# Kernel optimization log

Hardware: AMD Instinct MI355X
Metric: run time of the kernel (lower is better)

## Reference

```python
import jax, jax.numpy as jnp
import numpy as np

B, L, E, H, RR, BIO, NT, V, R = 16, 128, 256, 256, 128, 64, 3, 30000, 25


def setup_inputs() -> dict:
    key = jax.random.key(0)
    ks = jax.random.split(key, 24)
    s = 0.05
    n = jax.random.normal
    inp = {
        'tokens': jax.random.randint(ks[0], (B, L), 0, V),
        'bio_gold': jax.random.randint(ks[1], (B, L), 0, NT),
        'selection_gold': jax.random.uniform(ks[2], (B, L, R, L), jnp.float32),
        'word_emb': n(ks[3], (V, E), jnp.float32) * s,
        'W_ih_f': n(ks[4], (4 * H, E), jnp.float32) * s,
        'W_hh_f': n(ks[5], (4 * H, H), jnp.float32) * s,
        'b_f': n(ks[6], (4 * H,), jnp.float32) * s,
        'W_ih_b': n(ks[7], (4 * H, E), jnp.float32) * s,
        'W_hh_b': n(ks[8], (4 * H, H), jnp.float32) * s,
        'b_b': n(ks[9], (4 * H,), jnp.float32) * s,
        'emi_W': n(ks[10], (NT, H), jnp.float32) * s,
        'emi_b': n(ks[11], (NT,), jnp.float32) * s,
        'bio_emb': n(ks[12], (NT + 1, BIO), jnp.float32) * s,
        'sel_u_W': n(ks[13], (RR, H + BIO), jnp.float32) * s,
        'sel_u_b': n(ks[14], (RR,), jnp.float32) * s,
        'sel_v_W': n(ks[15], (RR, H + BIO), jnp.float32) * s,
        'sel_v_b': n(ks[16], (RR,), jnp.float32) * s,
        'sel_uv_W': n(ks[17], (RR, 2 * RR), jnp.float32) * s,
        'sel_uv_b': n(ks[18], (RR,), jnp.float32) * s,
        'rel_emb': n(ks[19], (R, RR), jnp.float32) * s,
        'crf_start': n(ks[20], (NT,), jnp.float32) * s,
        'crf_end': n(ks[21], (NT,), jnp.float32) * s,
        'crf_trans': n(ks[22], (NT, NT), jnp.float32) * s,
    }
    return inp


def _lstm(x, W_ih, W_hh, b, reverse):
    # x: [B,L,E] -> hidden states [B,L,H]; PyTorch gate order i,f,g,o
    Bb = x.shape[0]
    Hh = W_hh.shape[1]
    xg = jnp.swapaxes(jnp.einsum('ble,ge->blg', x, W_ih) + b, 0, 1)  # [L,B,4H]

    def step(carry, xt):
        h, c = carry
        g = xt + h @ W_hh.T
        i, f, gg, o = jnp.split(g, 4, axis=-1)
        c = jax.nn.sigmoid(f) * c + jax.nn.sigmoid(i) * jnp.tanh(gg)
        h = jax.nn.sigmoid(o) * jnp.tanh(c)
        return (h, c), h

    init = (jnp.zeros((Bb, Hh), x.dtype), jnp.zeros((Bb, Hh), x.dtype))
    _, hs = jax.lax.scan(step, init, xg, reverse=reverse)
    return jnp.swapaxes(hs, 0, 1)


def reference(tokens, bio_gold, selection_gold, word_emb, W_ih_f, W_hh_f, b_f,
              W_ih_b, W_hh_b, b_b, emi_W, emi_b, bio_emb, sel_u_W, sel_u_b,
              sel_v_W, sel_v_b, sel_uv_W, sel_uv_b, rel_emb, crf_start,
              crf_end, crf_trans):
    mask = tokens != 0  # pad id 0
    maskf = mask.astype(jnp.float32)
    emb = word_emb[tokens]
    # BiLSTM, halves averaged as in (fwd + bwd) / 2
    o = (_lstm(emb, W_ih_f, W_hh_f, b_f, False)
         + _lstm(emb, W_ih_b, W_hh_b, b_b, True)) * 0.5
    emi = o @ emi_W.T + emi_b  # [B,L,NT]

    # ---- CRF negative log-likelihood (torchcrf, reduction='mean') ----
    bidx = jnp.arange(tokens.shape[0])
    e_sel = jnp.take_along_axis(emi, bio_gold[..., None], axis=2)[..., 0]  # [B,L]
    num = crf_start[bio_gold[:, 0]] + e_sel[:, 0]
    tr = crf_trans[bio_gold[:, :-1], bio_gold[:, 1:]]  # [B,L-1]
    num = num + ((tr + e_sel[:, 1:]) * maskf[:, 1:]).sum(1)
    seq_ends = jnp.maximum(mask.sum(1) - 1, 0)
    num = num + crf_end[bio_gold[bidx, seq_ends]]

    def crf_step(score, inp):
        emi_t, m_t = inp
        nxt = jax.nn.logsumexp(score[:, :, None] + crf_trans[None] + emi_t[:, None, :], axis=1)
        return jnp.where(m_t[:, None], nxt, score), None

    score0 = crf_start + emi[:, 0]
    score, _ = jax.lax.scan(crf_step, score0,
                            (jnp.swapaxes(emi[:, 1:], 0, 1), jnp.swapaxes(mask[:, 1:], 0, 1)))
    den = jax.nn.logsumexp(score + crf_end, axis=1)
    crf_loss = -(num - den).mean()

    # ---- pairwise biaffine selection head ----
    oc = jnp.concatenate([o, bio_emb[bio_gold]], axis=-1)  # [B,L,H+BIO]
    u = jax.nn.relu(oc @ sel_u_W.T + sel_u_b)  # [B,L,RR]
    v = jax.nn.relu(oc @ sel_v_W.T + sel_v_b)
    Rr = rel_emb.shape[1]
    W1, W2 = sel_uv_W[:, :Rr], sel_uv_W[:, Rr:]  # split cat([u,v]) linear
    a = u @ W1.T  # indexed by j (u was expanded along dim 1)
    c = v @ W2.T  # indexed by i
    uv = jax.nn.relu(a[:, None, :, :] + c[:, :, None, :] + sel_uv_b)  # [B,L,L,RR]
    logits = jnp.einsum('bijh,rh->birj', uv, rel_emb)  # [B,L,R,L]

    y = selection_gold
    bce = jnp.maximum(logits, 0) - logits * y + jnp.log1p(jnp.exp(-jnp.abs(logits)))
    selmask = maskf[:, :, None, None] * maskf[:, None, None, :]  # [B,L,1,L]
    sel_loss = (bce * selmask).sum() / maskf.sum()
    return crf_loss + sel_loss
```

## Files before the change

kernel.cpp:

```cpp
#include <hip/hip_runtime.h>
#include <cstdint>
#include <cstddef>


typedef __attribute__((ext_vector_type(8))) short short8;
typedef __attribute__((ext_vector_type(8))) int i32x8;
typedef __attribute__((ext_vector_type(4))) float f32x4;

__device__ __forceinline__ unsigned short f2bf(float f) {
  unsigned int u = __float_as_uint(f);
  u += 0x7fffu + ((u >> 16) & 1u);
  return (unsigned short)(u >> 16);
}
__device__ __forceinline__ float bf2f(unsigned short u) {
  return __uint_as_float(((unsigned int)u) << 16);
}

__device__ __forceinline__ void dev_pp8k128(const float* __restrict__ W,
                                            unsigned int* __restrict__ out, int idx) {
  int c = idx & 3;
  int lane = (idx >> 2) & 63;
  int f = idx >> 8;
  int nt = f >> 1, kt = f & 1;
  int n = nt * 16 + (lane & 15);
  int k0 = kt * 128 + (lane >> 4) * 32 + c * 8;
  const float* wp = &W[(size_t)n * 256 + k0];
  int lo = 0, hi = 0;
  lo = __builtin_amdgcn_cvt_pk_fp8_f32(wp[0], wp[1], lo, false);
  lo = __builtin_amdgcn_cvt_pk_fp8_f32(wp[2], wp[3], lo, true);
  hi = __builtin_amdgcn_cvt_pk_fp8_f32(wp[4], wp[5], hi, false);
  hi = __builtin_amdgcn_cvt_pk_fp8_f32(wp[6], wp[7], hi, true);
  size_t base = ((size_t)(f << 6) + lane) * 8 + (c << 1);
  out[base] = (unsigned)lo;
  out[base + 1] = (unsigned)hi;
}

__device__ __forceinline__ void dev_ppw(const float* __restrict__ W, int ldw, int nkt,
                                        uint4* __restrict__ out, int idx) {
  int lane = idx & 63;
  int f = idx >> 6;
  int kt = f % nkt;
  int nt = f / nkt;
  int row = nt * 16 + (lane & 15);
  int k0 = kt * 32 + ((lane >> 4) << 3);
  const float* wp = &W[(size_t)row * ldw + k0];
  union { unsigned short us[8]; uint4 v; } tmp;
#pragma unroll
  for (int j = 0; j < 8; ++j) tmp.us[j] = f2bf(wp[j]);
  out[idx] = tmp.v;
}

__global__ __launch_bounds__(256) void k_setup(
    const float* __restrict__ Whhf, unsigned int* __restrict__ wpk8f,
    const float* __restrict__ Whhb, unsigned int* __restrict__ wpk8b,
    const float* __restrict__ Wihf, uint4* __restrict__ wihfPk,
    const float* __restrict__ Wihb, uint4* __restrict__ wihbPk,
    const float* __restrict__ suW, uint4* __restrict__ suPk,
    const float* __restrict__ svW, uint4* __restrict__ svPk,
    const float* __restrict__ suvW, uint4* __restrict__ w1Pk, uint4* __restrict__ w2Pk,
    float* __restrict__ acc) {
  int bid = blockIdx.x;
  int t = threadIdx.x;
  if (bid < 128) {
    dev_pp8k128(Whhf, wpk8f, bid * 256 + t);
  } else if (bid < 256) {
    dev_pp8k128(Whhb, wpk8b, (bid - 128) * 256 + t);
  } else if (bid < 384) {
    dev_ppw(Wihf, 256, 8, wihfPk, (bid - 256) * 256 + t);
  } else if (bid < 512) {
    dev_ppw(Wihb, 256, 8, wihbPk, (bid - 384) * 256 + t);
  } else if (bid < 532) {
    dev_ppw(suW, 320, 10, suPk, (bid - 512) * 256 + t);
  } else if (bid < 552) {
    dev_ppw(svW, 320, 10, svPk, (bid - 532) * 256 + t);
  } else if (bid < 560) {
    dev_ppw(suvW, 256, 4, w1Pk, (bid - 552) * 256 + t);
  } else if (bid < 568) {
    dev_ppw(suvW + 128, 256, 4, w2Pk, (bid - 560) * 256 + t);
  } else {
    if (t < 16) acc[t] = 0.f;
  }
}

__global__ __launch_bounds__(256) void k_xg(
    const int* __restrict__ tok, const float* __restrict__ wemb,
    const uint4* __restrict__ WpkF, const float* __restrict__ biasF,
    unsigned short* __restrict__ CF,
    const uint4* __restrict__ WpkB, const float* __restrict__ biasB,
    unsigned short* __restrict__ CB) {
  const uint4* Wp = blockIdx.z ? WpkB : WpkF;
  const float* bi = blockIdx.z ? biasB : biasF;
  unsigned short* Co = blockIdx.z ? CB : CF;
  int bn = blockIdx.x, bm = blockIdx.y;
  int tid = threadIdx.x;
  int w = tid >> 6;
  int lane = tid & 63;
  int m = lane & 15;
  int q = lane >> 4;
  int arow = bm * 64 + w * 16 + m;
  const float* ew = wemb + (size_t)tok[arow] * 256 + (q << 3);
  f32x4 z = {0.f, 0.f, 0.f, 0.f};
  f32x4 ac[4] = {z, z, z, z};
  for (int kt = 0; kt < 8; ++kt) {
    float4 e0 = *reinterpret_cast<const float4*>(ew + (kt << 5));
    float4 e1 = *reinterpret_cast<const float4*>(ew + (kt << 5) + 4);
    union { unsigned short us[8]; short8 v; } af;
    af.us[0] = f2bf(e0.x); af.us[1] = f2bf(e0.y); af.us[2] = f2bf(e0.z); af.us[3] = f2bf(e0.w);
    af.us[4] = f2bf(e1.x); af.us[5] = f2bf(e1.y); af.us[6] = f2bf(e1.z); af.us[7] = f2bf(e1.w);
#pragma unroll
    for (int nt = 0; nt < 4; ++nt) {
      uint4 b4 = Wp[(size_t)(((bn << 2) + nt) * 8 + kt) * 64 + lane];
      ac[nt] = __builtin_amdgcn_mfma_f32_16x16x32_bf16(af.v, __builtin_bit_cast(short8, b4), ac[nt], 0, 0, 0);
    }
  }
#pragma unroll
  for (int nt = 0; nt < 4; ++nt) {
    int col = (bn << 6) + (nt << 4) + m;
    float bv = bi[col];
#pragma unroll
    for (int reg = 0; reg < 4; ++reg) {
      int row = (bm << 6) + (w << 4) + (q << 2) + reg;
      Co[(size_t)row * 1024 + col] = f2bf(ac[nt][reg] + bv);
    }
  }
}

__global__ __launch_bounds__(1024, 4) void k_lstm8(
    const unsigned short* __restrict__ xgf, const unsigned short* __restrict__ xgb,
    const unsigned int* __restrict__ wpkf, const unsigned int* __restrict__ wpkb,
    unsigned short* __restrict__ hsf, unsigned short* __restrict__ hsb) {
  int bid = blockIdx.x;
  int dir = bid >> 4;
  int b = bid & 15;
  const unsigned short* xg = (dir ? xgb : xgf) + (size_t)b * 128 * 1024;
  const unsigned int* wpk = dir ? wpkb : wpkf;
  unsigned short* hseq = (dir ? hsb : hsf) + (size_t)b * 128 * 256;

  __shared__ __align__(16) unsigned short xgl[8 * 1024];
  __shared__ __align__(16) unsigned short hfl[8 * 256];
  __shared__ __align__(16) unsigned char h8[2][256];

  int tid = threadIdx.x;
  int w = tid >> 6;
  int lane = tid & 63;
  int m = lane & 15;
  int q = lane >> 4;

  i32x8 wfr[4][2];
#pragma unroll
  for (int g = 0; g < 4; ++g)
#pragma unroll
    for (int kt = 0; kt < 2; ++kt) {
      int f = (((g << 4) + w) << 1) + kt;
      wfr[g][kt] = *reinterpret_cast<const i32x8*>(wpk + (((size_t)(f << 6) + lane) << 3));
    }
#pragma unroll
  for (int g = 0; g < 4; ++g)
#pragma unroll
    for (int kt = 0; kt < 2; ++kt)
      asm volatile("" : "+v"(wfr[g][kt]));

  if (tid < 128) reinterpret_cast<unsigned int*>(&h8[0][0])[tid] = 0u;
  {
    int tb0 = dir ? 120 : 0;
    uint4 x0v = *reinterpret_cast<const uint4*>((const char*)xg + (size_t)tb0 * 2048 + tid * 16);
    reinterpret_cast<uint4*>(xgl)[tid] = x0v;
  }
  __syncthreads();

  float cstate = 0.f;
  int j = (w << 4) + m;

  for (int c = 0; c < 16; ++c) {
    int tbase = dir ? (120 - 8 * c) : (8 * c);
    uint4 xnext = {0, 0, 0, 0};
    if (c < 15) {
      int tb2 = dir ? (tbase - 8) : (tbase + 8);
      xnext = *reinterpret_cast<const uint4*>((const char*)xg + (size_t)tb2 * 2048 + tid * 16);
    }
#pragma unroll
    for (int i = 0; i < 8; ++i) {
      int s = 8 * c + i;
      int t = dir ? (127 - s) : s;
      int slot = t & 7;
      const unsigned char* cur = h8[s & 1];
      unsigned char* nxt = h8[(s & 1) ^ 1];

      const unsigned short* xb = xgl + slot * 1024 + j;
      float x0 = bf2f(xb[0]);
      float x1 = bf2f(xb[256]);
      float x2 = bf2f(xb[512]);
      float x3 = bf2f(xb[768]);

      i32x8 afr[2];
#pragma unroll
      for (int kt = 0; kt < 2; ++kt) {
        union { uint4 u[2]; i32x8 v; } tmp;
        const unsigned char* hp = cur + kt * 128 + q * 32;
        tmp.u[0] = *reinterpret_cast<const uint4*>(hp);
        tmp.u[1] = *reinterpret_cast<const uint4*>(hp + 16);
        afr[kt] = tmp.v;
      }

      f32x4 acg[4];
      acg[0] = (f32x4){x0, 0.f, 0.f, 0.f};
      acg[1] = (f32x4){x1, 0.f, 0.f, 0.f};
      acg[2] = (f32x4){x2, 0.f, 0.f, 0.f};
      acg[3] = (f32x4){x3, 0.f, 0.f, 0.f};
#pragma unroll
      for (int kt = 0; kt < 2; ++kt)
#pragma unroll
        for (int g = 0; g < 4; ++g)
          acg[g] = __builtin_amdgcn_mfma_scale_f32_16x16x128_f8f6f4(
              afr[kt], wfr[g][kt], acg[g],
              0, 0, 0, 0x7f7f7f7f, 0, 0x7f7f7f7f);

      float gi = acg[0][0];
      float gf = acg[1][0];
      float gg = acg[2][0];
      float go = acg[3][0];
      float si = __fdividef(1.f, 1.f + __expf(-gi));
      float sf = __fdividef(1.f, 1.f + __expf(-gf));
      float so = __fdividef(1.f, 1.f + __expf(-go));
      float tg = 1.f - __fdividef(2.f, __expf(2.f * gg) + 1.f);
      float cc2 = sf * cstate + si * tg;
      cstate = cc2;
      float th = 1.f - __fdividef(2.f, __expf(2.f * cc2) + 1.f);
      float h = so * th;
      if (q == 0) {
        hfl[slot * 256 + j] = f2bf(h);
        int pk = __builtin_amdgcn_cvt_pk_fp8_f32(h, h, 0, false);
        nxt[j] = (unsigned char)(pk & 0xff);
      }
      asm volatile("s_waitcnt lgkmcnt(0)" ::: "memory");
      __builtin_amdgcn_s_barrier();
      asm volatile("" ::: "memory");
    }
    if (tid < 256) {
      int trow = tid >> 5;
      int j0 = (tid & 31) << 3;
      uint4 hv = reinterpret_cast<const uint4*>(hfl)[tid];
      *reinterpret_cast<uint4*>(hseq + (size_t)(tbase + trow) * 256 + j0) = hv;
    }
    if (c < 15) {
      reinterpret_cast<uint4*>(xgl)[tid] = xnext;
      __syncthreads();
    }
  }
}

__global__ __launch_bounds__(256) void k_mid2(
    const unsigned short* __restrict__ hf16, const unsigned short* __restrict__ hb16,
    const int* __restrict__ bio, const float* __restrict__ bioE,
    const float* __restrict__ emiW, const float* __restrict__ emib,
    const uint4* __restrict__ suPk, const float* __restrict__ sub,
    const uint4* __restrict__ svPk, const float* __restrict__ svb,
    const uint4* __restrict__ w1Pk, const uint4* __restrict__ w2Pk,
    unsigned short* __restrict__ a16, unsigned short* __restrict__ c16,
    float* __restrict__ emi) {
  __shared__ __align__(16) unsigned short oc[16][328];
  __shared__ __align__(16) unsigned short ub[16][136];
  __shared__ __align__(16) unsigned short vb[16][136];
  int r0 = blockIdx.x * 16;
  int tid = threadIdx.x;

#pragma unroll
  for (int it = 0; it < 8; ++it) {
    int i = it * 256 + tid;
    int row = i >> 7, h2 = (i & 127) << 1;
    unsigned int af = *reinterpret_cast<const unsigned int*>(hf16 + (size_t)(r0 + row) * 256 + h2);
    unsigned int ab = *reinterpret_cast<const unsigned int*>(hb16 + (size_t)(r0 + row) * 256 + h2);
    float lo = 0.5f * (bf2f((unsigned short)af) + bf2f((unsigned short)ab));
    float hi = 0.5f * (bf2f((unsigned short)(af >> 16)) + bf2f((unsigned short)(ab >> 16)));
    unsigned int pk = (unsigned int)f2bf(lo) | ((unsigned int)f2bf(hi) << 16);
    *reinterpret_cast<unsigned int*>(&oc[row][h2]) = pk;
  }
#pragma unroll
  for (int it = 0; it < 2; ++it) {
    int i = it * 256 + tid;
    int row = i >> 5, p = (i & 31) << 1;
    int bi = bio[r0 + row];
    float b0 = bioE[bi * 64 + p], b1 = bioE[bi * 64 + p + 1];
    unsigned int pk = (unsigned int)f2bf(b0) | ((unsigned int)f2bf(b1) << 16);
    *reinterpret_cast<unsigned int*>(&oc[row][256 + p]) = pk;
  }
  __syncthreads();

  if (tid < 192) {
    int did = tid >> 2, sub4 = tid & 3;
    int row = did / 3, g = did - row * 3;
    const float* ew = emiW + g * 256 + sub4 * 64;
    float av = 0.f;
#pragma unroll
    for (int k = 0; k < 64; ++k) av += bf2f(oc[row][sub4 * 64 + k]) * ew[k];
    av += __shfl_xor(av, 1);
    av += __shfl_xor(av, 2);
    if (sub4 == 0) emi[(size_t)(r0 + row) * 3 + g] = av + emib[g];
  }

  int w = tid >> 6, lane = tid & 63, m = lane & 15, q = lane >> 4;
  {
    f32x4 z = {0.f, 0.f, 0.f, 0.f};
    f32x4 au[2] = {z, z}, av2[2] = {z, z};
    for (int kt = 0; kt < 10; ++kt) {
      uint4 a4 = *reinterpret_cast<const uint4*>(&oc[m][(kt << 5) + (q << 3)]);
      short8 af = __builtin_bit_cast(short8, a4);
#pragma unroll
      for (int d = 0; d < 2; ++d) {
        int nt = (w << 1) + d;
        uint4 bu = suPk[(size_t)(nt * 10 + kt) * 64 + lane];
        uint4 bv = svPk[(size_t)(nt * 10 + kt) * 64 + lane];
        au[d] = __builtin_amdgcn_mfma_f32_16x16x32_bf16(af, __builtin_bit_cast(short8, bu), au[d], 0, 0, 0);
        av2[d] = __builtin_amdgcn_mfma_f32_16x16x32_bf16(af, __builtin_bit_cast(short8, bv), av2[d], 0, 0, 0);
      }
    }
#pragma unroll
    for (int d = 0; d < 2; ++d) {
      int col = ((w << 1) + d) * 16 + m;
      float bu = sub[col], bv = svb[col];
#pragma unroll
      for (int reg = 0; reg < 4; ++reg) {
        int row = (q << 2) + reg;
        ub[row][col] = f2bf(fmaxf(au[d][reg] + bu, 0.f));
        vb[row][col] = f2bf(fmaxf(av2[d][reg] + bv, 0.f));
      }
    }
  }
  __syncthreads();

  {
    f32x4 z = {0.f, 0.f, 0.f, 0.f};
    f32x4 aa[2] = {z, z}, cc[2] = {z, z};
    for (int kt = 0; kt < 4; ++kt) {
      uint4 ua = *reinterpret_cast<const uint4*>(&ub[m][(kt << 5) + (q << 3)]);
      uint4 va = *reinterpret_cast<const uint4*>(&vb[m][(kt << 5) + (q << 3)]);
      short8 uf = __builtin_bit_cast(short8, ua);
      short8 vf = __builtin_bit_cast(short8, va);
#pragma unroll
      for (int d = 0; d < 2; ++d) {
        int nt = (w << 1) + d;
        uint4 b1 = w1Pk[(size_t)((nt << 2) + kt) * 64 + lane];
        uint4 b2 = w2Pk[(size_t)((nt << 2) + kt) * 64 + lane];
        aa[d] = __builtin_amdgcn_mfma_f32_16x16x32_bf16(uf, __builtin_bit_cast(short8, b1), aa[d], 0, 0, 0);
        cc[d] = __builtin_amdgcn_mfma_f32_16x16x32_bf16(vf, __builtin_bit_cast(short8, b2), cc[d], 0, 0, 0);
      }
    }
#pragma unroll
    for (int d = 0; d < 2; ++d) {
      int col = ((w << 1) + d) * 16 + m;
#pragma unroll
      for (int reg = 0; reg < 4; ++reg) {
        int row = r0 + (q << 2) + reg;
        a16[(size_t)row * 128 + col] = f2bf(aa[d][reg]);
        c16[(size_t)row * 128 + col] = f2bf(cc[d][reg]);
      }
    }
  }
}

__global__ __launch_bounds__(256) void k_loss(
    const unsigned short* __restrict__ a16, const unsigned short* __restrict__ c16,
    const float* __restrict__ suvb, const float* __restrict__ rel,
    const float* __restrict__ y, const int* __restrict__ tok,
    const float* __restrict__ emi, const int* __restrict__ bio,
    const float* __restrict__ cstart, const float* __restrict__ cend,
    const float* __restrict__ ctrans,
    float* __restrict__ acc, float* __restrict__ out) {
  int blk = blockIdx.x;
  int tid = threadIdx.x;
  if (blk < 1024) {
    __shared__ unsigned short alds[128][136];
    __shared__ float cbs[2][128];
    __shared__ float red[4];
    int b = blk >> 6;
    int ip = blk & 63;
    int hh = tid & 127;
    int half = tid >> 7;
#pragma unroll
    for (int it = 0; it < 32; ++it) {
      int idx = it * 256 + tid;
      int jrow = idx >> 6;
      int h2 = (idx & 63) << 1;
      unsigned int av = *reinterpret_cast<const unsigned int*>(
          a16 + ((size_t)(b << 7) + jrow) * 128 + h2);
      alds[h2][jrow] = (unsigned short)av;
      alds[h2 + 1][jrow] = (unsigned short)(av >> 16);
    }
    {
      int i = (ip << 1) + half;
      cbs[half][hh] = bf2f(c16[(size_t)((b << 7) + i) * 128 + hh]) + suvb[hh];
    }
    __syncthreads();
    int i = (ip << 1) + half;
    int j = hh;
    float lg[25];
#pragma unroll
    for (int r = 0; r < 25; ++r) lg[r] = 0.f;
    for (int h = 0; h < 128; ++h) {
      float av = bf2f(alds[h][j]);
      float uv = fmaxf(av + cbs[half][h], 0.f);
#pragma unroll
      for (int r = 0; r < 25; ++r) lg[r] += uv * rel[r * 128 + h];
    }
    float mi = (tok[(b << 7) + i] != 0) ? 1.f : 0.f;
    float mj = (tok[(b << 7) + j] != 0) ? 1.f : 0.f;
    const float* yp = y + (size_t)((b << 7) + i) * 3200 + j;
    float bs = 0.f;
#pragma unroll
    for (int r = 0; r < 25; ++r) {
      float x = lg[r];
      float yv = yp[r * 128];
      bs += fmaxf(x, 0.f) - x * yv + __logf(1.f + __expf(-fabsf(x)));
    }
    bs *= mi * mj;
#pragma unroll
    for (int off = 32; off; off >>= 1) bs += __shfl_down(bs, off);
    if ((tid & 63) == 0) red[tid >> 6] = bs;
    __syncthreads();
    if (tid == 0) atomicAdd(&acc[0], red[0] + red[1] + red[2] + red[3]);
  } else {
    __shared__ float elds[128][4];
    __shared__ float msk[128];
    __shared__ int biol[128];
    __shared__ float r_t[2], r_m[2];
    int b = blk - 1024;
    int t = tid;
    if (t < 128) {
      biol[t] = bio[b * 128 + t];
      msk[t] = (tok[b * 128 + t] != 0) ? 1.f : 0.f;
#pragma unroll
      for (int g = 0; g < 3; ++g) elds[t][g] = emi[(b * 128 + t) * 3 + g];
    }
    __syncthreads();
    if (t < 128) {
      float m = msk[t];
      float term;
      if (t == 0)
        term = cstart[biol[0]] + elds[0][biol[0]];
      else
        term = (ctrans[biol[t - 1] * 3 + biol[t]] + elds[t][biol[t]]) * m;
      float ms = m;
#pragma unroll
      for (int off = 32; off; off >>= 1) {
        term += __shfl_down(term, off);
        ms += __shfl_down(ms, off);
      }
      if ((t & 63) == 0) { r_t[t >> 6] = term; r_m[t >> 6] = ms; }
    }
    __syncthreads();
    if (t == 0) {
      float num = r_t[0] + r_t[1];
      float msum = r_m[0] + r_m[1];
      int se = (int)msum - 1;
      if (se < 0) se = 0;
      num += cend[biol[se]];
      float tr[9];
#pragma unroll
      for (int i2 = 0; i2 < 9; ++i2) tr[i2] = ctrans[i2];
      float s0 = cstart[0] + elds[0][0];
      float s1 = cstart[1] + elds[0][1];
      float s2 = cstart[2] + elds[0][2];
      for (int tt = 1; tt < 128; ++tt) {
        float a0, a1, a2, mx, n0, n1, n2;
        a0 = s0 + tr[0]; a1 = s1 + tr[3]; a2 = s2 + tr[6];
        mx = fmaxf(a0, fmaxf(a1, a2));
        n0 = mx + __logf(__expf(a0 - mx) + __expf(a1 - mx) + __expf(a2 - mx)) + elds[tt][0];
        a0 = s0 + tr[1]; a1 = s1 + tr[4]; a2 = s2 + tr[7];
        mx = fmaxf(a0, fmaxf(a1, a2));
        n1 = mx + __logf(__expf(a0 - mx) + __expf(a1 - mx) + __expf(a2 - mx)) + elds[tt][1];
        a0 = s0 + tr[2]; a1 = s1 + tr[5]; a2 = s2 + tr[8];
        mx = fmaxf(a0, fmaxf(a1, a2));
        n2 = mx + __logf(__expf(a0 - mx) + __expf(a1 - mx) + __expf(a2 - mx)) + elds[tt][2];
        if (msk[tt] != 0.f) { s0 = n0; s1 = n1; s2 = n2; }
      }
      float a0 = s0 + cend[0], a1 = s1 + cend[1], a2 = s2 + cend[2];
      float mx = fmaxf(a0, fmaxf(a1, a2));
      float den = mx + __logf(__expf(a0 - mx) + __expf(a1 - mx) + __expf(a2 - mx));
      atomicAdd(&acc[1], num - den);
      atomicAdd(&acc[2], msum);
    }
  }
  if (tid == 0) {
    __threadfence();
    unsigned old = atomicAdd((unsigned int*)(acc + 5), 1u);
    if (old == 1039u) {
      __threadfence();
      float s0 = atomicAdd(&acc[0], 0.f);
      float s1 = atomicAdd(&acc[1], 0.f);
      float s2 = atomicAdd(&acc[2], 0.f);
      out[0] = -(s1 * (1.f / 16.f)) + s0 / s2;
    }
  }
}

extern "C" void kernel_launch(void* const* d_in, const int* in_sizes, int n_in,
                              void* d_out, int out_size, void* d_ws, size_t ws_size,
                              hipStream_t stream) {
  const int* tokens = (const int*)d_in[0];
  const int* bio = (const int*)d_in[1];
  const float* selg = (const float*)d_in[2];
  const float* wemb = (const float*)d_in[3];
  const float* Wihf = (const float*)d_in[4];
  const float* Whhf = (const float*)d_in[5];
  const float* bf = (const float*)d_in[6];
  const float* Wihb = (const float*)d_in[7];
  const float* Whhb = (const float*)d_in[8];
  const float* bb = (const float*)d_in[9];
  const float* emiW = (const float*)d_in[10];
  const float* emib = (const float*)d_in[11];
  const float* bioE = (const float*)d_in[12];
  const float* suW = (const float*)d_in[13];
  const float* sub = (const float*)d_in[14];
  const float* svW = (const float*)d_in[15];
  const float* svb = (const float*)d_in[16];
  const float* suvW = (const float*)d_in[17];
  const float* suvb = (const float*)d_in[18];
  const float* rel = (const float*)d_in[19];
  const float* cstart = (const float*)d_in[20];
  const float* cend = (const float*)d_in[21];
  const float* ctrans = (const float*)d_in[22];

  float* ws = (float*)d_ws;
  float* xgf16 = ws;
  float* xgb16 = xgf16 + 1048576;
  float* hf16 = xgb16 + 1048576;
  float* hb16 = hf16 + 262144;
  float* a16 = hb16 + 262144;
  float* c16 = a16 + 131072;
  float* emi = c16 + 131072;
  float* wpk8f = emi + 6144;
  float* wpk8b = wpk8f + 65536;
  float* wihfPk = wpk8b + 65536;
  float* wihbPk = wihfPk + 131072;
  float* suPk = wihbPk + 131072;
  float* svPk = suPk + 20480;
  float* w1Pk = svPk + 20480;
  float* w2Pk = w1Pk + 8192;
  float* acc = w2Pk + 8192;

  k_setup<<<569, 256, 0, stream>>>(
      Whhf, (unsigned int*)wpk8f, Whhb, (unsigned int*)wpk8b,
      Wihf, (uint4*)wihfPk, Wihb, (uint4*)wihbPk,
      suW, (uint4*)suPk, svW, (uint4*)svPk,
      suvW, (uint4*)w1Pk, (uint4*)w2Pk, acc);

  k_xg<<<dim3(16, 32, 2), 256, 0, stream>>>(
      tokens, wemb,
      (const uint4*)wihfPk, bf, (unsigned short*)xgf16,
      (const uint4*)wihbPk, bb, (unsigned short*)xgb16);

  k_lstm8<<<32, 1024, 0, stream>>>(
      (const unsigned short*)xgf16, (const unsigned short*)xgb16,
      (const unsigned int*)wpk8f, (const unsigned int*)wpk8b,
      (unsigned short*)hf16, (unsigned short*)hb16);

  k_mid2<<<128, 256, 0, stream>>>(
      (const unsigned short*)hf16, (const unsigned short*)hb16,
      bio, bioE, emiW, emib,
      (const uint4*)suPk, sub, (const uint4*)svPk, svb,
      (const uint4*)w1Pk, (const uint4*)w2Pk,
      (unsigned short*)a16, (unsigned short*)c16, emi);

  k_loss<<<1040, 256, 0, stream>>>((const unsigned short*)a16, (const unsigned short*)c16,
                                   suvb, rel, selg, tokens, emi, bio,
                                   cstart, cend, ctrans, acc, (float*)d_out);
}
```

Before: 380.5 us.

## Halve LSTM block size, each wave computes two hidden-column tiles

The recurrent LSTM kernel now runs 512 threads (8 waves) per block instead of 1024, and each wave owns two 16-column tiles of the hidden state, holding twice the FP8 weight fragments in registers. The x-projection is added after the MFMAs instead of being used as the accumulator seed, and the xg prefetch is split into two loads per thread. The aim is to cut per-step barrier cost across fewer waves and give each wave more independent MFMAs to hide latency. The cost is higher register pressure per thread and more serial work per wave on each timestep.

```diff
diff --git a/kernel.cpp b/kernel.cpp
--- a/kernel.cpp
+++ b/kernel.cpp
@@ -125,7 +125,7 @@
   }
 }
 
-__global__ __launch_bounds__(1024, 4) void k_lstm8(
+__global__ __launch_bounds__(512, 2) void k_lstm8(
     const unsigned short* __restrict__ xgf, const unsigned short* __restrict__ xgb,
     const unsigned int* __restrict__ wpkf, const unsigned int* __restrict__ wpkb,
     unsigned short* __restrict__ hsf, unsigned short* __restrict__ hsb) {
@@ -146,37 +146,49 @@
   int m = lane & 15;
   int q = lane >> 4;
 
-  i32x8 wfr[4][2];
+  i32x8 wfr[4][2][2];
 #pragma unroll
   for (int g = 0; g < 4; ++g)
 #pragma unroll
-    for (int kt = 0; kt < 2; ++kt) {
-      int f = (((g << 4) + w) << 1) + kt;
-      wfr[g][kt] = *reinterpret_cast<const i32x8*>(wpk + (((size_t)(f << 6) + lane) << 3));
-    }
+    for (int n = 0; n < 2; ++n)
+#pragma unroll
+      for (int kt = 0; kt < 2; ++kt) {
+        int f = (((g << 4) + (w << 1) + n) << 1) + kt;
+        wfr[g][n][kt] = *reinterpret_cast<const i32x8*>(wpk + (((size_t)(f << 6) + lane) << 3));
+      }
 #pragma unroll
   for (int g = 0; g < 4; ++g)
 #pragma unroll
-    for (int kt = 0; kt < 2; ++kt)
-      asm volatile("" : "+v"(wfr[g][kt]));
+    for (int n = 0; n < 2; ++n)
+#pragma unroll
+      for (int kt = 0; kt < 2; ++kt)
+        asm volatile("" : "+v"(wfr[g][n][kt]));
 
   if (tid < 128) reinterpret_cast<unsigned int*>(&h8[0][0])[tid] = 0u;
   {
     int tb0 = dir ? 120 : 0;
-    uint4 x0v = *reinterpret_cast<const uint4*>((const char*)xg + (size_t)tb0 * 2048 + tid * 16);
-    reinterpret_cast<uint4*>(xgl)[tid] = x0v;
+#pragma unroll
+    for (int r2 = 0; r2 < 2; ++r2) {
+      uint4 x0v = *reinterpret_cast<const uint4*>(
+          (const char*)xg + (size_t)tb0 * 2048 + (size_t)(tid + (r2 << 9)) * 16);
+      reinterpret_cast<uint4*>(xgl)[tid + (r2 << 9)] = x0v;
+    }
   }
   __syncthreads();
 
-  float cstate = 0.f;
-  int j = (w << 4) + m;
+  const f32x4 zero4 = {0.f, 0.f, 0.f, 0.f};
+  float cst[2] = {0.f, 0.f};
+  int j0 = (w << 5) + m;
 
   for (int c = 0; c < 16; ++c) {
     int tbase = dir ? (120 - 8 * c) : (8 * c);
-    uint4 xnext = {0, 0, 0, 0};
+    uint4 xnext0 = {0, 0, 0, 0}, xnext1 = {0, 0, 0, 0};
     if (c < 15) {
       int tb2 = dir ? (tbase - 8) : (tbase + 8);
-      xnext = *reinterpret_cast<const uint4*>((const char*)xg + (size_t)tb2 * 2048 + tid * 16);
+      xnext0 = *reinterpret_cast<const uint4*>(
+          (const char*)xg + (size_t)tb2 * 2048 + (size_t)tid * 16);
+      xnext1 = *reinterpret_cast<const uint4*>(
+          (const char*)xg + (size_t)tb2 * 2048 + (size_t)(tid + 512) * 16);
     }
 #pragma unroll
     for (int i = 0; i < 8; ++i) {
@@ -186,12 +198,6 @@
       const unsigned char* cur = h8[s & 1];
       unsigned char* nxt = h8[(s & 1) ^ 1];
 
-      const unsigned short* xb = xgl + slot * 1024 + j;
-      float x0 = bf2f(xb[0]);
-      float x1 = bf2f(xb[256]);
-      float x2 = bf2f(xb[512]);
-      float x3 = bf2f(xb[768]);
-
       i32x8 afr[2];
 #pragma unroll
       for (int kt = 0; kt < 2; ++kt) {
@@ -202,35 +208,45 @@
         afr[kt] = tmp.v;
       }
 
-      f32x4 acg[4];
-      acg[0] = (f32x4){x0, 0.f, 0.f, 0.f};
-      acg[1] = (f32x4){x1, 0.f, 0.f, 0.f};
-      acg[2] = (f32x4){x2, 0.f, 0.f, 0.f};
-      acg[3] = (f32x4){x3, 0.f, 0.f, 0.f};
-#pragma unroll
-      for (int kt = 0; kt < 2; ++kt)
+      float xv[4][2];
+#pragma unroll
+      for (int g = 0; g < 4; ++g)
+#pragma unroll
+        for (int n = 0; n < 2; ++n)
+          xv[g][n] = bf2f(xgl[slot * 1024 + (g << 8) + j0 + (n << 4)]);
+
+      f32x4 acg[4][2];
+#pragma unroll
+      for (int n = 0; n < 2; ++n) {
 #pragma unroll
         for (int g = 0; g < 4; ++g)
-          acg[g] = __builtin_amdgcn_mfma_scale_f32_16x16x128_f8f6f4(
-              afr[kt], wfr[g][kt], acg[g],
-              0, 0, 0, 0x7f7f7f7f, 0, 0x7f7f7f7f);
-
-      float gi = acg[0][0];
-      float gf = acg[1][0];
-      float gg = acg[2][0];
-      float go = acg[3][0];
-      float si = __fdividef(1.f, 1.f + __expf(-gi));
-      float sf = __fdividef(1.f, 1.f + __expf(-gf));
-      float so = __fdividef(1.f, 1.f + __expf(-go));
-      float tg = 1.f - __fdividef(2.f, __expf(2.f * gg) + 1.f);
-      float cc2 = sf * cstate + si * tg;
-      cstate = cc2;
-      float th = 1.f - __fdividef(2.f, __expf(2.f * cc2) + 1.f);
-      float h = so * th;
-      if (q == 0) {
-        hfl[slot * 256 + j] = f2bf(h);
-        int pk = __builtin_amdgcn_cvt_pk_fp8_f32(h, h, 0, false);
-        nxt[j] = (unsigned char)(pk & 0xff);
+          acg[g][n] = __builtin_amdgcn_mfma_scale_f32_16x16x128_f8f6f4(
+              afr[0], wfr[g][n][0], zero4, 0, 0, 0, 0x7f7f7f7f, 0, 0x7f7f7f7f);
+#pragma unroll
+        for (int g = 0; g < 4; ++g)
+          acg[g][n] = __builtin_amdgcn_mfma_scale_f32_16x16x128_f8f6f4(
+              afr[1], wfr[g][n][1], acg[g][n], 0, 0, 0, 0x7f7f7f7f, 0, 0x7f7f7f7f);
+      }
+
+#pragma unroll
+      for (int n = 0; n < 2; ++n) {
+        float gi = acg[0][n][0] + xv[0][n];
+        float gf = acg[1][n][0] + xv[1][n];
+        float gg = acg[2][n][0] + xv[2][n];
+        float go = acg[3][n][0] + xv[3][n];
+        float si = __fdividef(1.f, 1.f + __expf(-gi));
+        float sf = __fdividef(1.f, 1.f + __expf(-gf));
+        float so = __fdividef(1.f, 1.f + __expf(-go));
+        float tg = 1.f - __fdividef(2.f, __expf(2.f * gg) + 1.f);
+        float cc = sf * cst[n] + si * tg;
+        cst[n] = cc;
+        float th = 1.f - __fdividef(2.f, __expf(2.f * cc) + 1.f);
+        float h = so * th;
+        if (q == 0) {
+          hfl[slot * 256 + j0 + (n << 4)] = f2bf(h);
+          int pk = __builtin_amdgcn_cvt_pk_fp8_f32(h, h, 0, false);
+          nxt[j0 + (n << 4)] = (unsigned char)(pk & 0xff);
+        }
       }
       asm volatile("s_waitcnt lgkmcnt(0)" ::: "memory");
       __builtin_amdgcn_s_barrier();
@@ -238,12 +254,13 @@
     }
     if (tid < 256) {
       int trow = tid >> 5;
-      int j0 = (tid & 31) << 3;
+      int jf = (tid & 31) << 3;
       uint4 hv = reinterpret_cast<const uint4*>(hfl)[tid];
-      *reinterpret_cast<uint4*>(hseq + (size_t)(tbase + trow) * 256 + j0) = hv;
+      *reinterpret_cast<uint4*>(hseq + (size_t)(tbase + trow) * 256 + jf) = hv;
     }
     if (c < 15) {
-      reinterpret_cast<uint4*>(xgl)[tid] = xnext;
+      reinterpret_cast<uint4*>(xgl)[tid] = xnext0;
+      reinterpret_cast<uint4*>(xgl)[tid + 512] = xnext1;
       __syncthreads();
     }
   }
@@ -549,7 +566,7 @@
       (const uint4*)wihfPk, bf, (unsigned short*)xgf16,
       (const uint4*)wihbPk, bb, (unsigned short*)xgb16);
 
-  k_lstm8<<<32, 1024, 0, stream>>>(
+  k_lstm8<<<32, 512, 0, stream>>>(
       (const unsigned short*)xgf16, (const unsigned short*)xgb16,
       (const unsigned int*)wpk8f, (const unsigned int*)wpk8b,
       (unsigned short*)hf16, (unsigned short*)hb16);
```

After: 394.2 us. 1.04x slower.
